# Performance work log

Measured on AMD Instinct MI355X. Metric: run time of the kernel, lower is better.

## Reference

```python
import jax, jax.numpy as jnp
import numpy as np

D = 768          # 16*16*3
N = 196
H = 8
HD = D // H      # 96
SCALE = HD ** -0.5
EPS = 1e-5


def _ln(x, s, b):
    m = jnp.mean(x, axis=-1, keepdims=True)
    v = jnp.mean((x - m) ** 2, axis=-1, keepdims=True)
    return (x - m) * jax.lax.rsqrt(v + EPS) * s + b


def setup_inputs() -> dict:
    key = jax.random.key(0)
    ks = jax.random.split(key, 16)
    B = 64
    w = lambda k, shp: (jax.random.normal(k, shp, jnp.float32) * 0.02)
    return {
        "x": jax.random.normal(ks[0], (B, N, D), jnp.float32),
        "x_Eem": jax.random.normal(ks[1], (B, 3, 222, 222), jnp.float32),
        "pos_emb": jax.random.normal(ks[2], (1, N, D), jnp.float32),
        "dw_w": w(ks[3], (3, 1, 16, 16)),     # depthwise conv, groups=3 (OIHW, I=1)
        "dw_b": jnp.zeros((3,), jnp.float32),
        "pw_w": w(ks[4], (D, 3)),             # pointwise 1x1 conv as matrix
        "pw_b": jnp.zeros((D,), jnp.float32),
        "qkv_w": w(ks[5], (3 * D, D)),        # no bias (qkv_bias=False)
        "proj_w": w(ks[6], (D, D)),
        "proj_b": jnp.zeros((D,), jnp.float32),
        "ln1_s": jnp.ones((D,), jnp.float32),
        "ln1_b": jnp.zeros((D,), jnp.float32),
        "ln2_s": jnp.ones((D,), jnp.float32),
        "ln2_b": jnp.zeros((D,), jnp.float32),
        "fc1_w": w(ks[7], (4 * D, D)),
        "fc1_b": jnp.zeros((4 * D,), jnp.float32),
        "fc2_w": w(ks[8], (D, 4 * D)),
        "fc2_b": jnp.zeros((D,), jnp.float32),
    }


def _patch_embed(img, dw_w, dw_b, pw_w, pw_b):
    # depthwise conv: kernel 16, stride 16, padding 1, groups=3
    h = jax.lax.conv_general_dilated(
        img, dw_w, window_strides=(16, 16), padding=[(1, 1), (1, 1)],
        dimension_numbers=("NCHW", "OIHW", "NCHW"), feature_group_count=3)
    h = h + dw_b[None, :, None, None]           # [B,3,14,14]
    h = jnp.einsum("bchw,oc->bohw", h, pw_w) + pw_b[None, :, None, None]
    B = h.shape[0]
    return h.reshape(B, D, N).transpose(0, 2, 1)  # [B,N,D]


def _ve_attention(x, x_emb, qkv_w, proj_w, proj_b):
    B = x.shape[0]
    # pooling gates (AdaptiveMax/AvgPool2d on 3D input pools last two dims)
    maxg = jnp.max(x, axis=(1, 2), keepdims=True)       # [B,1,1]
    maxn = jnp.max(x, axis=2, keepdims=True)            # [B,N,1]
    aveg = jnp.mean(x, axis=(1, 2), keepdims=True)      # [B,1,1]
    aven = jnp.mean(x, axis=2, keepdims=True)           # [B,N,1]
    # F.softmax(maxg*maxn, dim=1); F.softmax(aveg*aven) -> default dim=0 for 3D input
    gate = jax.nn.softmax(maxg * maxn, axis=1) * jax.nn.softmax(aveg * aven, axis=0)
    qkv = jnp.einsum("bnd,ed->bne", x, qkv_w)            # [B,N,3D]
    q = qkv[:, :, :D]
    k = qkv[:, :, D:2 * D]
    v = qkv[:, :, 2 * D:] * gate + x_emb
    to_h = lambda t: t.reshape(B, N, H, HD).transpose(0, 2, 1, 3)  # [B,H,N,hd]
    q, k, v = to_h(q), to_h(k), to_h(v)
    # scores = (q@k^T + v@k^T) * scale == ((q+v)@k^T) * scale
    attn = jax.nn.softmax(jnp.einsum("bhnd,bhmd->bhnm", q + v, k) * SCALE, axis=-1)
    out = jnp.einsum("bhnm,bhmd->bhnd", attn, v)
    out = out.transpose(0, 2, 1, 3).reshape(B, N, D)
    return jnp.einsum("bnd,ed->bne", out, proj_w) + proj_b


def reference(x, x_Eem, pos_emb, dw_w, dw_b, pw_w, pw_b, qkv_w, proj_w, proj_b,
              ln1_s, ln1_b, ln2_s, ln2_b, fc1_w, fc1_b, fc2_w, fc2_b):
    x_emb = _patch_embed(x_Eem, dw_w, dw_b, pw_w, pw_b)
    x = x + pos_emb
    x = x + _ve_attention(_ln(x, ln1_s, ln1_b), x_emb, qkv_w, proj_w, proj_b)
    h = _ln(x, ln2_s, ln2_b)
    h = jax.nn.gelu(jnp.einsum("bnd,fd->bnf", h, fc1_w) + fc1_b, approximate=False)
    h = jnp.einsum("bnf,df->bnd", h, fc2_w) + fc2_b
    return x + h
```

## Files before the change

### kernel.cpp

```cpp
#include <hip/hip_runtime.h>

#define DEV __device__ __forceinline__

typedef __attribute__((ext_vector_type(8))) short short8_t;
typedef __attribute__((ext_vector_type(4))) float float4_t;
typedef __attribute__((ext_vector_type(4))) unsigned short ushort4_t;
typedef __attribute__((ext_vector_type(8))) unsigned short ushort8_t;

#define ATT_SCALE 0.10206207261596577f

DEV unsigned short f2bf(float f) {
  unsigned u = __float_as_uint(f);
  u += 0x7fffu + ((u >> 16) & 1u);
  return (unsigned short)(u >> 16);
}
DEV float bf2f(unsigned short h) { return __uint_as_float(((unsigned)h) << 16); }

DEV float4_t mfma16(short8_t a, short8_t b, float4_t c) {
  return __builtin_amdgcn_mfma_f32_16x16x32_bf16(a, b, c, 0, 0, 0);
}

DEV void gl_lds16(const void* g, void* l) {
  __builtin_amdgcn_global_load_lds((__attribute__((address_space(1))) void*)g,
                                   (__attribute__((address_space(3))) void*)l, 16, 0, 0);
}

__global__ __launch_bounds__(256) void cvt_kernel(const float* __restrict__ w0,
    const float* __restrict__ w1, const float* __restrict__ w2, const float* __restrict__ w3,
    unsigned short* __restrict__ d0, unsigned short* __restrict__ d1,
    unsigned short* __restrict__ d2, unsigned short* __restrict__ d3) {
  const int i = blockIdx.x * 256 + threadIdx.x;
  const float* s;
  unsigned short* d;
  int j;
  if (i < 442368) { s = w0; d = d0; j = i; }
  else if (i < 589824) { s = w1; d = d1; j = i - 442368; }
  else if (i < 1179648) { s = w2; d = d2; j = i - 589824; }
  else { s = w3; d = d3; j = i - 1179648; }
  float4_t v = ((const float4_t*)s)[j];
  ushort4_t o = {f2bf(v[0]), f2bf(v[1]), f2bf(v[2]), f2bf(v[3])};
  ((ushort4_t*)d)[j] = o;
}

__global__ __launch_bounds__(256) void dwconv_kernel(const float* __restrict__ img,
    const float* __restrict__ wgt, const float* __restrict__ wb, float* __restrict__ h3) {
  __shared__ float wsm[256];
  const int bc = blockIdx.x;
  const int c = bc % 3;
  const int tid = threadIdx.x;
  wsm[tid] = wgt[c * 256 + tid];
  __syncthreads();
  if (tid < 196) {
    const int ph = tid / 14, pwv = tid % 14;
    const float* ip = img + (size_t)bc * (222 * 222);
    float acc = 0.f;
#pragma unroll
    for (int i = 0; i < 16; ++i) {
      const int r = ph * 16 - 1 + i;
      if ((unsigned)r < 222u) {
        const float* rp = ip + r * 222;
#pragma unroll
        for (int j = 0; j < 16; ++j) {
          const int cc = pwv * 16 - 1 + j;
          if ((unsigned)cc < 222u) acc += rp[cc] * wsm[i * 16 + j];
        }
      }
    }
    h3[(size_t)bc * 196 + tid] = acc + wb[c];
  }
}

__global__ __launch_bounds__(256) void ln1_kernel(const float* __restrict__ x,
    const float* __restrict__ pos, const float* __restrict__ sG, const float* __restrict__ bG,
    unsigned short* __restrict__ xln, float* __restrict__ maxn, float* __restrict__ aven) {
  __shared__ float rA[4], rB[4], rC[4], rD[4];
  const int row = blockIdx.x, tid = threadIdx.x;
  const int n = row % 196;
  const float* xr = x + (size_t)row * 768;
  const float* pr = pos + (size_t)n * 768;
  float v0 = xr[tid] + pr[tid];
  float v1 = xr[tid + 256] + pr[tid + 256];
  float v2 = xr[tid + 512] + pr[tid + 512];
  float sm = v0 + v1 + v2;
  float sq = v0 * v0 + v1 * v1 + v2 * v2;
  for (int o = 32; o; o >>= 1) { sm += __shfl_xor(sm, o); sq += __shfl_xor(sq, o); }
  if ((tid & 63) == 0) { rA[tid >> 6] = sm; rB[tid >> 6] = sq; }
  __syncthreads();
  const float mean = (rA[0] + rA[1] + rA[2] + rA[3]) * (1.f / 768.f);
  const float var = (rB[0] + rB[1] + rB[2] + rB[3]) * (1.f / 768.f) - mean * mean;
  const float rstd = rsqrtf(var + 1e-5f);
  float y0 = (v0 - mean) * rstd * sG[tid] + bG[tid];
  float y1 = (v1 - mean) * rstd * sG[tid + 256] + bG[tid + 256];
  float y2 = (v2 - mean) * rstd * sG[tid + 512] + bG[tid + 512];
  unsigned short* xo = xln + (size_t)row * 768;
  xo[tid] = f2bf(y0); xo[tid + 256] = f2bf(y1); xo[tid + 512] = f2bf(y2);
  float mx = fmaxf(y0, fmaxf(y1, y2));
  float sy = y0 + y1 + y2;
  for (int o = 32; o; o >>= 1) { mx = fmaxf(mx, __shfl_xor(mx, o)); sy += __shfl_xor(sy, o); }
  if ((tid & 63) == 0) { rC[tid >> 6] = mx; rD[tid >> 6] = sy; }
  __syncthreads();
  if (tid == 0) {
    maxn[row] = fmaxf(fmaxf(rC[0], rC[1]), fmaxf(rC[2], rC[3]));
    aven[row] = (rD[0] + rD[1] + rD[2] + rD[3]) * (1.f / 768.f);
  }
}

__global__ __launch_bounds__(256) void ln2_kernel(const float* __restrict__ x2,
    const float* __restrict__ sG, const float* __restrict__ bG, unsigned short* __restrict__ h2) {
  __shared__ float rA[4], rB[4];
  const int row = blockIdx.x, tid = threadIdx.x;
  const float* xr = x2 + (size_t)row * 768;
  float v0 = xr[tid], v1 = xr[tid + 256], v2 = xr[tid + 512];
  float sm = v0 + v1 + v2;
  float sq = v0 * v0 + v1 * v1 + v2 * v2;
  for (int o = 32; o; o >>= 1) { sm += __shfl_xor(sm, o); sq += __shfl_xor(sq, o); }
  if ((tid & 63) == 0) { rA[tid >> 6] = sm; rB[tid >> 6] = sq; }
  __syncthreads();
  const float mean = (rA[0] + rA[1] + rA[2] + rA[3]) * (1.f / 768.f);
  const float var = (rB[0] + rB[1] + rB[2] + rB[3]) * (1.f / 768.f) - mean * mean;
  const float rstd = rsqrtf(var + 1e-5f);
  unsigned short* xo = h2 + (size_t)row * 768;
  xo[tid]       = f2bf((v0 - mean) * rstd * sG[tid] + bG[tid]);
  xo[tid + 256] = f2bf((v1 - mean) * rstd * sG[tid + 256] + bG[tid + 256]);
  xo[tid + 512] = f2bf((v2 - mean) * rstd * sG[tid + 512] + bG[tid + 512]);
}

__global__ __launch_bounds__(256) void gate1_kernel(const float* __restrict__ maxn,
    const float* __restrict__ aven, float* __restrict__ aveg, float* __restrict__ s1) {
  __shared__ float rA[4], rB[4], rC[4], rD[4];
  const int b = blockIdx.x, tid = threadIdx.x;
  const bool ok = tid < 196;
  const float mv = ok ? maxn[b * 196 + tid] : -1e30f;
  const float av = ok ? aven[b * 196 + tid] : 0.f;
  float m = mv, sa = av;
  for (int o = 32; o; o >>= 1) { m = fmaxf(m, __shfl_xor(m, o)); sa += __shfl_xor(sa, o); }
  if ((tid & 63) == 0) { rA[tid >> 6] = m; rB[tid >> 6] = sa; }
  __syncthreads();
  const float maxg = fmaxf(fmaxf(rA[0], rA[1]), fmaxf(rA[2], rA[3]));
  const float avg = (rB[0] + rB[1] + rB[2] + rB[3]) * (1.f / 196.f);
  if (tid == 0) aveg[b] = avg;
  const float t1 = ok ? maxg * mv : -1e30f;
  float m2 = t1;
  for (int o = 32; o; o >>= 1) m2 = fmaxf(m2, __shfl_xor(m2, o));
  if ((tid & 63) == 0) rC[tid >> 6] = m2;
  __syncthreads();
  const float m2g = fmaxf(fmaxf(rC[0], rC[1]), fmaxf(rC[2], rC[3]));
  const float e = ok ? __expf(t1 - m2g) : 0.f;
  float se = e;
  for (int o = 32; o; o >>= 1) se += __shfl_xor(se, o);
  if ((tid & 63) == 0) rD[tid >> 6] = se;
  __syncthreads();
  const float seg = rD[0] + rD[1] + rD[2] + rD[3];
  if (ok) s1[b * 196 + tid] = e / seg;
}

__global__ __launch_bounds__(64) void gate2_kernel(const float* __restrict__ aveg,
    const float* __restrict__ aven, const float* __restrict__ s1, float* __restrict__ gate) {
  const int n = blockIdx.x, bb = threadIdx.x;
  const float t2 = aveg[bb] * aven[bb * 196 + n];
  float m = t2;
  for (int o = 32; o; o >>= 1) m = fmaxf(m, __shfl_xor(m, o));
  const float e = __expf(t2 - m);
  float ssum = e;
  for (int o = 32; o; o >>= 1) ssum += __shfl_xor(ssum, o);
  gate[bb * 196 + n] = s1[bb * 196 + n] * e / ssum;
}

enum { M_QKV = 0, M_PROJ = 1, M_GELU = 2, M_FC2 = 3 };

template <int MODE>
__global__ __launch_bounds__(256, 2) void gemm_bt(
    const unsigned short* __restrict__ A, const unsigned short* __restrict__ W,
    int K, int Nd, int NT, int T,
    const float* __restrict__ bias,
    const float* __restrict__ res0, const float* __restrict__ res1,
    const float* __restrict__ gate, const float* __restrict__ h3,
    const float* __restrict__ pw, const float* __restrict__ pwb,
    unsigned short* __restrict__ oQ, unsigned short* __restrict__ oK,
    unsigned short* __restrict__ oV,
    float* __restrict__ oF, unsigned short* __restrict__ oB) {
  __shared__ __align__(16) unsigned short smem[16384];
  const int l = blockIdx.x;
  const int xc = l & 7, kb = l >> 3;
  const int tbase = (xc * T) >> 3;
  if (kb >= (((xc + 1) * T) >> 3) - tbase) return;
  const int t = tbase + kb;
  const int mt = t / NT, nt = t - mt * NT;
  const int m0 = mt * 128, n0 = nt * 128;

  const int tid = threadIdx.x;
  const int w = tid >> 6, lane = tid & 63;
  const int l15 = lane & 15, quad = lane >> 4;

  const int srow = w * 8 + (lane >> 3);
  const int cs = (lane & 7) ^ (lane >> 3);
  size_t aoff[4], boff[4];
#pragma unroll
  for (int j = 0; j < 4; ++j) {
    aoff[j] = (size_t)(m0 + j * 32 + srow) * K + cs * 8;
    boff[j] = (size_t)(n0 + j * 32 + srow) * K + cs * 8;
  }
  char* sb = (char*)smem;

  float4_t acc[4][4];
#pragma unroll
  for (int i = 0; i < 4; ++i)
#pragma unroll
    for (int j = 0; j < 4; ++j) acc[i][j] = (float4_t){0.f, 0.f, 0.f, 0.f};

  const int wm = (w >> 1) << 6, wn = (w & 1) << 6;
  const unsigned short* as_ = smem;
  const unsigned short* bs_ = smem + 8192;
  const int rx = l15 & 7;

  for (int kt = 0; kt < K; kt += 64) {
#pragma unroll
    for (int j = 0; j < 4; ++j) gl_lds16(A + aoff[j] + kt, sb + j * 4096 + w * 1024);
#pragma unroll
    for (int j = 0; j < 4; ++j) gl_lds16(W + boff[j] + kt, sb + 16384 + j * 4096 + w * 1024);
    __syncthreads();
#pragma unroll
    for (int h = 0; h < 2; ++h) {
      const int ch = (quad + 4 * h) ^ rx;
      short8_t af[4], bfr[4];
#pragma unroll
      for (int mi = 0; mi < 4; ++mi)
        af[mi] = *(const short8_t*)(as_ + (wm + mi * 16 + l15) * 64 + ch * 8);
#pragma unroll
      for (int ni = 0; ni < 4; ++ni)
        bfr[ni] = *(const short8_t*)(bs_ + (wn + ni * 16 + l15) * 64 + ch * 8);
#pragma unroll
      for (int mi = 0; mi < 4; ++mi)
#pragma unroll
        for (int ni = 0; ni < 4; ++ni)
          acc[mi][ni] = mfma16(bfr[ni], af[mi], acc[mi][ni]);
    }
    __syncthreads();
  }

  if (MODE == M_QKV) {
    const int sel = n0 / 768;
    unsigned short* dst = (sel == 0) ? oQ : (sel == 1) ? oK : oV;
    const int nb = n0 - sel * 768 + wn;
#pragma unroll
    for (int mi = 0; mi < 4; ++mi) {
      const int m = m0 + wm + mi * 16 + l15;
      float gv = 0.f, h30 = 0.f, h31 = 0.f, h32 = 0.f;
      if (sel == 2) {
        const int b = m / 196, n = m - b * 196;
        gv = gate[m];
        h30 = h3[(b * 3 + 0) * 196 + n];
        h31 = h3[(b * 3 + 1) * 196 + n];
        h32 = h3[(b * 3 + 2) * 196 + n];
      }
      unsigned short* orow = dst + (size_t)m * 768;
#pragma unroll
      for (int ni = 0; ni < 4; ++ni) {
        const int dcol = nb + ni * 16 + quad * 4;
        ushort4_t st;
        if (sel == 2) {
          const float4_t pwf0 = *(const float4_t*)(pw + dcol * 3);
          const float4_t pwf1 = *(const float4_t*)(pw + dcol * 3 + 4);
          const float4_t pwf2 = *(const float4_t*)(pw + dcol * 3 + 8);
          const float4_t pbf = *(const float4_t*)(pwb + dcol);
          float pwflat[12] = {pwf0[0], pwf0[1], pwf0[2], pwf0[3], pwf1[0], pwf1[1],
                              pwf1[2], pwf1[3], pwf2[0], pwf2[1], pwf2[2], pwf2[3]};
#pragma unroll
          for (int r = 0; r < 4; ++r) {
            const float v = acc[mi][ni][r] * gv + h30 * pwflat[3 * r] +
                            h31 * pwflat[3 * r + 1] + h32 * pwflat[3 * r + 2] + pbf[r];
            st[r] = f2bf(v);
          }
        } else {
#pragma unroll
          for (int r = 0; r < 4; ++r) st[r] = f2bf(acc[mi][ni][r]);
        }
        *(ushort4_t*)(orow + dcol) = st;
      }
    }
  } else if (MODE == M_PROJ || MODE == M_FC2) {
#pragma unroll
    for (int mi = 0; mi < 4; ++mi) {
      const int m = m0 + wm + mi * 16 + l15;
      const int nseq = m % 196;
      const float* rr0 = res0 + (size_t)m * 768;
      const float* rr1 = (MODE == M_PROJ) ? res1 + (size_t)nseq * 768 : nullptr;
      float* oo = oF + (size_t)m * 768;
#pragma unroll
      for (int ni = 0; ni < 4; ++ni) {
        const int col = n0 + wn + ni * 16 + quad * 4;
        const float4_t bb = *(const float4_t*)(bias + col);
        const float4_t r0v = *(const float4_t*)(rr0 + col);
        float4_t v;
#pragma unroll
        for (int r = 0; r < 4; ++r) v[r] = acc[mi][ni][r] + bb[r] + r0v[r];
        if (MODE == M_PROJ) {
          const float4_t r1v = *(const float4_t*)(rr1 + col);
#pragma unroll
          for (int r = 0; r < 4; ++r) v[r] += r1v[r];
        }
        *(float4_t*)(oo + col) = v;
      }
    }
  } else {
#pragma unroll
    for (int mi = 0; mi < 4; ++mi) {
      const int m = m0 + wm + mi * 16 + l15;
      unsigned short* oo = oB + (size_t)m * Nd;
#pragma unroll
      for (int ni = 0; ni < 4; ++ni) {
        const int col = n0 + wn + ni * 16 + quad * 4;
        const float4_t bb = *(const float4_t*)(bias + col);
        ushort4_t st;
#pragma unroll
        for (int r = 0; r < 4; ++r) {
          const float t2 = acc[mi][ni][r] + bb[r];
          st[r] = f2bf(0.5f * t2 * (1.f + erff(t2 * 0.70710678118654752f)));
        }
        *(ushort4_t*)(oo + col) = st;
      }
    }
  }
}

__global__ __launch_bounds__(256) void vtrans_kernel(const unsigned short* __restrict__ vg,
                                                     unsigned short* __restrict__ vt) {
  __shared__ unsigned short lds[96 * 226];
  const int bh = blockIdx.x, b = bh >> 3, h = bh & 7;
  const int tid = threadIdx.x;
  const unsigned short* base = vg + (size_t)(b * 196) * 768 + h * 96;
  for (int idx = tid; idx < 196 * 12; idx += 256) {
    const int n = idx / 12, c = idx % 12;
    const ushort8_t rv = *(const ushort8_t*)(base + (size_t)n * 768 + c * 8);
#pragma unroll
    for (int j = 0; j < 8; ++j) lds[(c * 8 + j) * 226 + n] = rv[j];
  }
  __syncthreads();
  unsigned short* ob = vt + (size_t)bh * (96 * 224);
  for (int idx = tid; idx < 96 * 28; idx += 256) {
    const int d = idx / 28, c = idx % 28;
    const int nn = c * 8;
    ushort8_t o;
#pragma unroll
    for (int j = 0; j < 8; ++j) o[j] = (nn + j < 196) ? lds[d * 226 + nn + j] : (unsigned short)0;
    *(ushort8_t*)(ob + (size_t)d * 224 + nn) = o;
  }
}

__global__ __launch_bounds__(256, 2) void attn_kernel(
    const unsigned short* __restrict__ qg, const unsigned short* __restrict__ vg,
    const unsigned short* __restrict__ kg, const unsigned short* __restrict__ vt,
    unsigned short* __restrict__ att) {
  __shared__ __align__(16) unsigned short p_s[4][16][232];
  const int tid = threadIdx.x, w = tid >> 6, lane = tid & 63;
  const int l15 = lane & 15, quad = lane >> 4;
  const int l = blockIdx.x;
  const int bt = (l & 7) * 208 + (l >> 3);
  const int t = bt * 4 + w;
  const int bh = t / 13, qt = t - bh * 13;
  const int b = bh >> 3, h = bh & 7;
  const unsigned short* qb = qg + (size_t)(b * 196) * 768 + h * 96;
  const unsigned short* vb = vg + (size_t)(b * 196) * 768 + h * 96;
  const unsigned short* kb = kg + (size_t)(b * 196) * 768 + h * 96;
  const unsigned short* vtb = vt + (size_t)bh * (96 * 224);
  for (int i = lane; i < 256; i += 64) p_s[w][i >> 4][208 + (i & 15)] = 0;

  const size_t qoff = (size_t)(qt * 16 + l15) * 768 + quad * 8;
  short8_t a0, a1, a2;
  {
    const ushort8_t q0 = *(const ushort8_t*)(qb + qoff);
    const ushort8_t q1 = *(const ushort8_t*)(qb + qoff + 32);
    const ushort8_t q2 = *(const ushort8_t*)(qb + qoff + 64);
    const ushort8_t v0 = *(const ushort8_t*)(vb + qoff);
    const ushort8_t v1 = *(const ushort8_t*)(vb + qoff + 32);
    const ushort8_t v2 = *(const ushort8_t*)(vb + qoff + 64);
#pragma unroll
    for (int j = 0; j < 8; ++j) {
      a0[j] = (short)f2bf(bf2f(q0[j]) + bf2f(v0[j]));
      a1[j] = (short)f2bf(bf2f(q1[j]) + bf2f(v1[j]));
      a2[j] = (short)f2bf(bf2f(q2[j]) + bf2f(v2[j]));
    }
  }
  float4_t S[13];
#pragma unroll
  for (int c = 0; c < 13; ++c) S[c] = (float4_t){0.f, 0.f, 0.f, 0.f};
#pragma unroll
  for (int c = 0; c < 13; ++c) {
    const unsigned short* kr = kb + (size_t)(c * 16 + l15) * 768 + quad * 8;
    S[c] = mfma16(a0, *(const short8_t*)(kr), S[c]);
    S[c] = mfma16(a1, *(const short8_t*)(kr + 32), S[c]);
    S[c] = mfma16(a2, *(const short8_t*)(kr + 64), S[c]);
  }
  float mx[4] = {-1e30f, -1e30f, -1e30f, -1e30f};
#pragma unroll
  for (int c = 0; c < 13; ++c) {
    const bool okc = (c * 16 + l15) < 196;
#pragma unroll
    for (int r = 0; r < 4; ++r) {
      const float v = S[c][r] * ATT_SCALE;
      S[c][r] = okc ? v : -1e30f;
      mx[r] = fmaxf(mx[r], S[c][r]);
    }
  }
#pragma unroll
  for (int o = 1; o <= 8; o <<= 1)
#pragma unroll
    for (int r = 0; r < 4; ++r) mx[r] = fmaxf(mx[r], __shfl_xor(mx[r], o));
  float sum[4] = {0.f, 0.f, 0.f, 0.f};
#pragma unroll
  for (int c = 0; c < 13; ++c)
#pragma unroll
    for (int r = 0; r < 4; ++r) {
      const float e = __expf(S[c][r] - mx[r]);
      S[c][r] = e;
      sum[r] += e;
    }
#pragma unroll
  for (int o = 1; o <= 8; o <<= 1)
#pragma unroll
    for (int r = 0; r < 4; ++r) sum[r] += __shfl_xor(sum[r], o);
  float inv[4];
#pragma unroll
  for (int r = 0; r < 4; ++r) inv[r] = 1.f / sum[r];
#pragma unroll
  for (int c = 0; c < 13; ++c)
#pragma unroll
    for (int r = 0; r < 4; ++r)
      p_s[w][quad * 4 + r][c * 16 + l15] = f2bf(S[c][r] * inv[r]);

  float4_t O[6];
#pragma unroll
  for (int ni = 0; ni < 6; ++ni) O[ni] = (float4_t){0.f, 0.f, 0.f, 0.f};
#pragma unroll
  for (int s = 0; s < 7; ++s) {
    short8_t pa = *(const short8_t*)(&p_s[w][l15][s * 32 + quad * 8]);
#pragma unroll
    for (int ni = 0; ni < 6; ++ni) {
      short8_t vf = *(const short8_t*)(vtb + (size_t)(ni * 16 + l15) * 224 + s * 32 + quad * 8);
      O[ni] = mfma16(vf, pa, O[ni]);
    }
  }
#pragma unroll
  for (int ni = 0; ni < 6; ++ni) {
    ushort4_t st = {f2bf(O[ni][0]), f2bf(O[ni][1]), f2bf(O[ni][2]), f2bf(O[ni][3])};
    *(ushort4_t*)(&p_s[w][l15][ni * 16 + quad * 4]) = st;
  }
  __asm__ volatile("s_waitcnt lgkmcnt(0)");
  unsigned short* ab = att + (size_t)(b * 196) * 768 + h * 96;
#pragma unroll
  for (int p = 0; p < 3; ++p) {
    const int idx = p * 64 + lane;
    const int row = idx / 12, c16 = idx - row * 12;
    const int m = qt * 16 + row;
    if (m < 196) {
      const ushort8_t o = *(const ushort8_t*)(&p_s[w][row][c16 * 8]);
      *(ushort8_t*)(ab + (size_t)m * 768 + c16 * 8) = o;
    }
  }
}

extern "C" void kernel_launch(void* const* d_in, const int* in_sizes, int n_in,
                              void* d_out, int out_size, void* d_ws, size_t ws_size,
                              hipStream_t stream) {
  (void)in_sizes; (void)n_in; (void)out_size; (void)ws_size;
  const float* x      = (const float*)d_in[0];
  const float* xE     = (const float*)d_in[1];
  const float* pos    = (const float*)d_in[2];
  const float* dw_w   = (const float*)d_in[3];
  const float* dw_b   = (const float*)d_in[4];
  const float* pw_w   = (const float*)d_in[5];
  const float* pw_b   = (const float*)d_in[6];
  const float* qkv_w  = (const float*)d_in[7];
  const float* proj_w = (const float*)d_in[8];
  const float* proj_b = (const float*)d_in[9];
  const float* ln1_s  = (const float*)d_in[10];
  const float* ln1_b  = (const float*)d_in[11];
  const float* ln2_s  = (const float*)d_in[12];
  const float* ln2_b  = (const float*)d_in[13];
  const float* fc1_w  = (const float*)d_in[14];
  const float* fc1_b  = (const float*)d_in[15];
  const float* fc2_w  = (const float*)d_in[16];
  const float* fc2_b  = (const float*)d_in[17];
  float* out = (float*)d_out;

  char* ws = (char*)d_ws;
  size_t off = 0;
  auto alloc = [&](size_t bytes) -> void* {
    void* p = ws + off;
    off += (bytes + 255) & ~(size_t)255;
    return p;
  };
  unsigned short* wqkv  = (unsigned short*)alloc(1769472ull * 2);
  unsigned short* wproj = (unsigned short*)alloc(589824ull * 2);
  unsigned short* wfc1  = (unsigned short*)alloc(2359296ull * 2);
  unsigned short* wfc2  = (unsigned short*)alloc(2359296ull * 2);
  float* h3   = (float*)alloc(37632ull * 4);
  unsigned short* xln = (unsigned short*)alloc(9633792ull * 2);
  float* maxn = (float*)alloc(12544ull * 4);
  float* aven = (float*)alloc(12544ull * 4);
  float* aveg = (float*)alloc(64ull * 4);
  float* s1   = (float*)alloc(12544ull * 4);
  float* gate = (float*)alloc(12544ull * 4);
  const size_t ROWP = 9646080ull;
  unsigned short* big = (unsigned short*)alloc((3ull * ROWP + 11010048ull) * 2);
  unsigned short* qg = big;
  unsigned short* kg = big + ROWP;
  unsigned short* vg = big + 2ull * ROWP;
  unsigned short* vt = big + 3ull * ROWP;
  unsigned short* att  = xln;
  unsigned short* h2   = xln;
  unsigned short* gbuf = big;
  float* x2 = out;

  cvt_kernel<<<dim3(6912), 256, 0, stream>>>(qkv_w, proj_w, fc1_w, fc2_w, wqkv, wproj, wfc1, wfc2);
  dwconv_kernel<<<dim3(192), 256, 0, stream>>>(xE, dw_w, dw_b, h3);
  ln1_kernel<<<dim3(12544), 256, 0, stream>>>(x, pos, ln1_s, ln1_b, xln, maxn, aven);
  gate1_kernel<<<dim3(64), 256, 0, stream>>>(maxn, aven, aveg, s1);
  gate2_kernel<<<dim3(196), 64, 0, stream>>>(aveg, aven, s1, gate);
  gemm_bt<M_QKV><<<dim3(1768), 256, 0, stream>>>(xln, wqkv, 768, 2304, 18, 1764,
      nullptr, nullptr, nullptr, gate, h3, pw_w, pw_b, qg, kg, vg, nullptr, nullptr);
  vtrans_kernel<<<dim3(512), 256, 0, stream>>>(vg, vt);
  attn_kernel<<<dim3(1664), 256, 0, stream>>>(qg, vg, kg, vt, att);
  gemm_bt<M_PROJ><<<dim3(592), 256, 0, stream>>>(att, wproj, 768, 768, 6, 588,
      proj_b, x, pos, nullptr, nullptr, nullptr, nullptr, nullptr, nullptr, nullptr, x2, nullptr);
  ln2_kernel<<<dim3(12544), 256, 0, stream>>>(x2, ln2_s, ln2_b, h2);
  gemm_bt<M_GELU><<<dim3(2352), 256, 0, stream>>>(h2, wfc1, 768, 3072, 24, 2352,
      fc1_b, nullptr, nullptr, nullptr, nullptr, nullptr, nullptr, nullptr, nullptr, nullptr,
      nullptr, gbuf);
  gemm_bt<M_FC2><<<dim3(592), 256, 0, stream>>>(gbuf, wfc2, 3072, 768, 6, 588,
      fc2_b, x2, nullptr, nullptr, nullptr, nullptr, nullptr, nullptr, nullptr, nullptr, out,
      nullptr);
}
```

Measured before the change: 520.3 us.

## Double-buffer GEMM LDS tiles with templated K-step and merge prep kernels

The GEMM main loop becomes double-buffered: the next K-tile is issued as an async global-to-LDS load while the current tile is being consumed, which drops one barrier per iteration. The K-tile width is now a template parameter, 32 for the QKV and FC1 GEMMs and 64 for proj and FC2, and the LDS swizzle is generalised to match. Separately, weight conversion, the depthwise conv and LN1 are merged into one launch to cut launch overhead. Double buffering doubles LDS use at BK=64, which may reduce occupancy, and the global_load_lds writes rely on the single barrier at the top of each iteration for ordering.

```diff
diff --git a/kernel.cpp b/kernel.cpp
--- a/kernel.cpp
+++ b/kernel.cpp
@@ -25,83 +25,86 @@
                                    (__attribute__((address_space(3))) void*)l, 16, 0, 0);
 }
 
-__global__ __launch_bounds__(256) void cvt_kernel(const float* __restrict__ w0,
-    const float* __restrict__ w1, const float* __restrict__ w2, const float* __restrict__ w3,
-    unsigned short* __restrict__ d0, unsigned short* __restrict__ d1,
-    unsigned short* __restrict__ d2, unsigned short* __restrict__ d3) {
-  const int i = blockIdx.x * 256 + threadIdx.x;
-  const float* s;
-  unsigned short* d;
-  int j;
-  if (i < 442368) { s = w0; d = d0; j = i; }
-  else if (i < 589824) { s = w1; d = d1; j = i - 442368; }
-  else if (i < 1179648) { s = w2; d = d2; j = i - 589824; }
-  else { s = w3; d = d3; j = i - 1179648; }
-  float4_t v = ((const float4_t*)s)[j];
-  ushort4_t o = {f2bf(v[0]), f2bf(v[1]), f2bf(v[2]), f2bf(v[3])};
-  ((ushort4_t*)d)[j] = o;
-}
-
-__global__ __launch_bounds__(256) void dwconv_kernel(const float* __restrict__ img,
-    const float* __restrict__ wgt, const float* __restrict__ wb, float* __restrict__ h3) {
-  __shared__ float wsm[256];
-  const int bc = blockIdx.x;
-  const int c = bc % 3;
-  const int tid = threadIdx.x;
-  wsm[tid] = wgt[c * 256 + tid];
-  __syncthreads();
-  if (tid < 196) {
-    const int ph = tid / 14, pwv = tid % 14;
-    const float* ip = img + (size_t)bc * (222 * 222);
-    float acc = 0.f;
-#pragma unroll
-    for (int i = 0; i < 16; ++i) {
-      const int r = ph * 16 - 1 + i;
-      if ((unsigned)r < 222u) {
-        const float* rp = ip + r * 222;
-#pragma unroll
-        for (int j = 0; j < 16; ++j) {
-          const int cc = pwv * 16 - 1 + j;
-          if ((unsigned)cc < 222u) acc += rp[cc] * wsm[i * 16 + j];
+__global__ __launch_bounds__(256) void prep_kernel(
+    const float* __restrict__ w0, const float* __restrict__ w1, const float* __restrict__ w2,
+    const float* __restrict__ w3, unsigned short* __restrict__ d0, unsigned short* __restrict__ d1,
+    unsigned short* __restrict__ d2, unsigned short* __restrict__ d3,
+    const float* __restrict__ img, const float* __restrict__ dwW, const float* __restrict__ dwB,
+    float* __restrict__ h3,
+    const float* __restrict__ x, const float* __restrict__ pos, const float* __restrict__ sG,
+    const float* __restrict__ bG, unsigned short* __restrict__ xln, float* __restrict__ maxn,
+    float* __restrict__ aven) {
+  __shared__ float sh[256];
+  const int blk = blockIdx.x, tid = threadIdx.x;
+  if (blk < 6912) {
+    const int i = blk * 256 + tid;
+    const float* s;
+    unsigned short* d;
+    int j;
+    if (i < 442368) { s = w0; d = d0; j = i; }
+    else if (i < 589824) { s = w1; d = d1; j = i - 442368; }
+    else if (i < 1179648) { s = w2; d = d2; j = i - 589824; }
+    else { s = w3; d = d3; j = i - 1179648; }
+    float4_t v = ((const float4_t*)s)[j];
+    ushort4_t o = {f2bf(v[0]), f2bf(v[1]), f2bf(v[2]), f2bf(v[3])};
+    ((ushort4_t*)d)[j] = o;
+  } else if (blk < 7104) {
+    const int bc = blk - 6912;
+    const int c = bc % 3;
+    sh[tid] = dwW[c * 256 + tid];
+    __syncthreads();
+    if (tid < 196) {
+      const int ph = tid / 14, pwv = tid % 14;
+      const float* ip = img + (size_t)bc * (222 * 222);
+      float acc = 0.f;
+#pragma unroll
+      for (int i = 0; i < 16; ++i) {
+        const int r = ph * 16 - 1 + i;
+        if ((unsigned)r < 222u) {
+          const float* rp = ip + r * 222;
+#pragma unroll
+          for (int j = 0; j < 16; ++j) {
+            const int cc = pwv * 16 - 1 + j;
+            if ((unsigned)cc < 222u) acc += rp[cc] * sh[i * 16 + j];
+          }
         }
       }
-    }
-    h3[(size_t)bc * 196 + tid] = acc + wb[c];
-  }
-}
-
-__global__ __launch_bounds__(256) void ln1_kernel(const float* __restrict__ x,
-    const float* __restrict__ pos, const float* __restrict__ sG, const float* __restrict__ bG,
-    unsigned short* __restrict__ xln, float* __restrict__ maxn, float* __restrict__ aven) {
-  __shared__ float rA[4], rB[4], rC[4], rD[4];
-  const int row = blockIdx.x, tid = threadIdx.x;
-  const int n = row % 196;
-  const float* xr = x + (size_t)row * 768;
-  const float* pr = pos + (size_t)n * 768;
-  float v0 = xr[tid] + pr[tid];
-  float v1 = xr[tid + 256] + pr[tid + 256];
-  float v2 = xr[tid + 512] + pr[tid + 512];
-  float sm = v0 + v1 + v2;
-  float sq = v0 * v0 + v1 * v1 + v2 * v2;
-  for (int o = 32; o; o >>= 1) { sm += __shfl_xor(sm, o); sq += __shfl_xor(sq, o); }
-  if ((tid & 63) == 0) { rA[tid >> 6] = sm; rB[tid >> 6] = sq; }
-  __syncthreads();
-  const float mean = (rA[0] + rA[1] + rA[2] + rA[3]) * (1.f / 768.f);
-  const float var = (rB[0] + rB[1] + rB[2] + rB[3]) * (1.f / 768.f) - mean * mean;
-  const float rstd = rsqrtf(var + 1e-5f);
-  float y0 = (v0 - mean) * rstd * sG[tid] + bG[tid];
-  float y1 = (v1 - mean) * rstd * sG[tid + 256] + bG[tid + 256];
-  float y2 = (v2 - mean) * rstd * sG[tid + 512] + bG[tid + 512];
-  unsigned short* xo = xln + (size_t)row * 768;
-  xo[tid] = f2bf(y0); xo[tid + 256] = f2bf(y1); xo[tid + 512] = f2bf(y2);
-  float mx = fmaxf(y0, fmaxf(y1, y2));
-  float sy = y0 + y1 + y2;
-  for (int o = 32; o; o >>= 1) { mx = fmaxf(mx, __shfl_xor(mx, o)); sy += __shfl_xor(sy, o); }
-  if ((tid & 63) == 0) { rC[tid >> 6] = mx; rD[tid >> 6] = sy; }
-  __syncthreads();
-  if (tid == 0) {
-    maxn[row] = fmaxf(fmaxf(rC[0], rC[1]), fmaxf(rC[2], rC[3]));
-    aven[row] = (rD[0] + rD[1] + rD[2] + rD[3]) * (1.f / 768.f);
+      h3[(size_t)bc * 196 + tid] = acc + dwB[c];
+    }
+  } else {
+    float* rA = sh;
+    float* rB = sh + 4;
+    float* rC = sh + 8;
+    float* rD = sh + 12;
+    const int row = blk - 7104;
+    const int n = row % 196;
+    const float* xr = x + (size_t)row * 768;
+    const float* pr = pos + (size_t)n * 768;
+    float v0 = xr[tid] + pr[tid];
+    float v1 = xr[tid + 256] + pr[tid + 256];
+    float v2 = xr[tid + 512] + pr[tid + 512];
+    float sm = v0 + v1 + v2;
+    float sq = v0 * v0 + v1 * v1 + v2 * v2;
+    for (int o = 32; o; o >>= 1) { sm += __shfl_xor(sm, o); sq += __shfl_xor(sq, o); }
+    if ((tid & 63) == 0) { rA[tid >> 6] = sm; rB[tid >> 6] = sq; }
+    __syncthreads();
+    const float mean = (rA[0] + rA[1] + rA[2] + rA[3]) * (1.f / 768.f);
+    const float var = (rB[0] + rB[1] + rB[2] + rB[3]) * (1.f / 768.f) - mean * mean;
+    const float rstd = rsqrtf(var + 1e-5f);
+    float y0 = (v0 - mean) * rstd * sG[tid] + bG[tid];
+    float y1 = (v1 - mean) * rstd * sG[tid + 256] + bG[tid + 256];
+    float y2 = (v2 - mean) * rstd * sG[tid + 512] + bG[tid + 512];
+    unsigned short* xo = xln + (size_t)row * 768;
+    xo[tid] = f2bf(y0); xo[tid + 256] = f2bf(y1); xo[tid + 512] = f2bf(y2);
+    float mx = fmaxf(y0, fmaxf(y1, y2));
+    float sy = y0 + y1 + y2;
+    for (int o = 32; o; o >>= 1) { mx = fmaxf(mx, __shfl_xor(mx, o)); sy += __shfl_xor(sy, o); }
+    if ((tid & 63) == 0) { rC[tid >> 6] = mx; rD[tid >> 6] = sy; }
+    __syncthreads();
+    if (tid == 0) {
+      maxn[row] = fmaxf(fmaxf(rC[0], rC[1]), fmaxf(rC[2], rC[3]));
+      aven[row] = (rD[0] + rD[1] + rD[2] + rD[3]) * (1.f / 768.f);
+    }
   }
 }
 
@@ -168,7 +171,7 @@
 
 enum { M_QKV = 0, M_PROJ = 1, M_GELU = 2, M_FC2 = 3 };
 
-template <int MODE>
+template <int MODE, int BK>
 __global__ __launch_bounds__(256, 2) void gemm_bt(
     const unsigned short* __restrict__ A, const unsigned short* __restrict__ W,
     int K, int Nd, int NT, int T,
@@ -179,7 +182,13 @@
     unsigned short* __restrict__ oQ, unsigned short* __restrict__ oK,
     unsigned short* __restrict__ oV,
     float* __restrict__ oF, unsigned short* __restrict__ oB) {
-  __shared__ __align__(16) unsigned short smem[16384];
+  constexpr int TE = 128 * BK;
+  constexpr int ABYTES = TE * 2;
+  constexpr int NCALL = ABYTES / 4096;
+  constexpr int RPC = 128 / NCALL;
+  constexpr int CH = BK / 8;
+  __shared__ __align__(16) unsigned short smem[4 * TE];
+
   const int l = blockIdx.x;
   const int xc = l & 7, kb = l >> 3;
   const int tbase = (xc * T) >> 3;
@@ -192,13 +201,13 @@
   const int w = tid >> 6, lane = tid & 63;
   const int l15 = lane & 15, quad = lane >> 4;
 
-  const int srow = w * 8 + (lane >> 3);
-  const int cs = (lane & 7) ^ (lane >> 3);
-  size_t aoff[4], boff[4];
-#pragma unroll
-  for (int j = 0; j < 4; ++j) {
-    aoff[j] = (size_t)(m0 + j * 32 + srow) * K + cs * 8;
-    boff[j] = (size_t)(n0 + j * 32 + srow) * K + cs * 8;
+  const int srow = w * (RPC / 4) + lane / CH;
+  const int sch = (lane % CH) ^ ((lane / CH) % CH);
+  size_t aoff[NCALL], boff[NCALL];
+#pragma unroll
+  for (int j = 0; j < NCALL; ++j) {
+    aoff[j] = (size_t)(m0 + j * RPC + srow) * K + sch * 8;
+    boff[j] = (size_t)(n0 + j * RPC + srow) * K + sch * 8;
   }
   char* sb = (char*)smem;
 
@@ -209,33 +218,45 @@
     for (int j = 0; j < 4; ++j) acc[i][j] = (float4_t){0.f, 0.f, 0.f, 0.f};
 
   const int wm = (w >> 1) << 6, wn = (w & 1) << 6;
-  const unsigned short* as_ = smem;
-  const unsigned short* bs_ = smem + 8192;
-  const int rx = l15 & 7;
-
-  for (int kt = 0; kt < K; kt += 64) {
-#pragma unroll
-    for (int j = 0; j < 4; ++j) gl_lds16(A + aoff[j] + kt, sb + j * 4096 + w * 1024);
-#pragma unroll
-    for (int j = 0; j < 4; ++j) gl_lds16(W + boff[j] + kt, sb + 16384 + j * 4096 + w * 1024);
+  const int NK = K / BK;
+
+#pragma unroll
+  for (int j = 0; j < NCALL; ++j) gl_lds16(A + aoff[j], sb + j * 4096 + w * 1024);
+#pragma unroll
+  for (int j = 0; j < NCALL; ++j) gl_lds16(W + boff[j], sb + ABYTES + j * 4096 + w * 1024);
+
+  for (int k = 0; k < NK; ++k) {
     __syncthreads();
-#pragma unroll
-    for (int h = 0; h < 2; ++h) {
-      const int ch = (quad + 4 * h) ^ rx;
+    if (k + 1 < NK) {
+      char* dst = sb + ((k + 1) & 1) * 2 * ABYTES;
+      const size_t ko = (size_t)(k + 1) * BK;
+#pragma unroll
+      for (int j = 0; j < NCALL; ++j) gl_lds16(A + aoff[j] + ko, dst + j * 4096 + w * 1024);
+#pragma unroll
+      for (int j = 0; j < NCALL; ++j)
+        gl_lds16(W + boff[j] + ko, dst + ABYTES + j * 4096 + w * 1024);
+    }
+    const unsigned short* as_ = smem + (k & 1) * 2 * TE;
+    const unsigned short* bs_ = as_ + TE;
+#pragma unroll
+    for (int h = 0; h < BK / 32; ++h) {
       short8_t af[4], bfr[4];
 #pragma unroll
-      for (int mi = 0; mi < 4; ++mi)
-        af[mi] = *(const short8_t*)(as_ + (wm + mi * 16 + l15) * 64 + ch * 8);
-#pragma unroll
-      for (int ni = 0; ni < 4; ++ni)
-        bfr[ni] = *(const short8_t*)(bs_ + (wn + ni * 16 + l15) * 64 + ch * 8);
+      for (int mi = 0; mi < 4; ++mi) {
+        const int r = wm + mi * 16 + l15;
+        af[mi] = *(const short8_t*)(as_ + r * BK + (((quad + 4 * h) ^ (r & (CH - 1))) * 8));
+      }
+#pragma unroll
+      for (int ni = 0; ni < 4; ++ni) {
+        const int r = wn + ni * 16 + l15;
+        bfr[ni] = *(const short8_t*)(bs_ + r * BK + (((quad + 4 * h) ^ (r & (CH - 1))) * 8));
+      }
 #pragma unroll
       for (int mi = 0; mi < 4; ++mi)
 #pragma unroll
         for (int ni = 0; ni < 4; ++ni)
           acc[mi][ni] = mfma16(bfr[ni], af[mi], acc[mi][ni]);
     }
-    __syncthreads();
   }
 
   if (MODE == M_QKV) {
@@ -512,22 +533,21 @@
   unsigned short* gbuf = big;
   float* x2 = out;
 
-  cvt_kernel<<<dim3(6912), 256, 0, stream>>>(qkv_w, proj_w, fc1_w, fc2_w, wqkv, wproj, wfc1, wfc2);
-  dwconv_kernel<<<dim3(192), 256, 0, stream>>>(xE, dw_w, dw_b, h3);
-  ln1_kernel<<<dim3(12544), 256, 0, stream>>>(x, pos, ln1_s, ln1_b, xln, maxn, aven);
+  prep_kernel<<<dim3(19648), 256, 0, stream>>>(qkv_w, proj_w, fc1_w, fc2_w, wqkv, wproj, wfc1,
+      wfc2, xE, dw_w, dw_b, h3, x, pos, ln1_s, ln1_b, xln, maxn, aven);
   gate1_kernel<<<dim3(64), 256, 0, stream>>>(maxn, aven, aveg, s1);
   gate2_kernel<<<dim3(196), 64, 0, stream>>>(aveg, aven, s1, gate);
-  gemm_bt<M_QKV><<<dim3(1768), 256, 0, stream>>>(xln, wqkv, 768, 2304, 18, 1764,
+  gemm_bt<M_QKV, 32><<<dim3(1768), 256, 0, stream>>>(xln, wqkv, 768, 2304, 18, 1764,
       nullptr, nullptr, nullptr, gate, h3, pw_w, pw_b, qg, kg, vg, nullptr, nullptr);
   vtrans_kernel<<<dim3(512), 256, 0, stream>>>(vg, vt);
   attn_kernel<<<dim3(1664), 256, 0, stream>>>(qg, vg, kg, vt, att);
-  gemm_bt<M_PROJ><<<dim3(592), 256, 0, stream>>>(att, wproj, 768, 768, 6, 588,
+  gemm_bt<M_PROJ, 64><<<dim3(592), 256, 0, stream>>>(att, wproj, 768, 768, 6, 588,
       proj_b, x, pos, nullptr, nullptr, nullptr, nullptr, nullptr, nullptr, nullptr, x2, nullptr);
   ln2_kernel<<<dim3(12544), 256, 0, stream>>>(x2, ln2_s, ln2_b, h2);
-  gemm_bt<M_GELU><<<dim3(2352), 256, 0, stream>>>(h2, wfc1, 768, 3072, 24, 2352,
+  gemm_bt<M_GELU, 32><<<dim3(2352), 256, 0, stream>>>(h2, wfc1, 768, 3072, 24, 2352,
       fc1_b, nullptr, nullptr, nullptr, nullptr, nullptr, nullptr, nullptr, nullptr, nullptr,
       nullptr, gbuf);
-  gemm_bt<M_FC2><<<dim3(592), 256, 0, stream>>>(gbuf, wfc2, 3072, 768, 6, 588,
+  gemm_bt<M_FC2, 64><<<dim3(592), 256, 0, stream>>>(gbuf, wfc2, 3072, 768, 6, 588,
       fc2_b, x2, nullptr, nullptr, nullptr, nullptr, nullptr, nullptr, nullptr, nullptr, out,
       nullptr);
 }
```

Measured after the change: 579.7 us. +11.4%, slower.
